# Kernel optimization log

Measured on AMD Instinct MI355X. Metric: run time of the kernel, lower is better.

## Reference

```python
import jax, jax.numpy as jnp
import numpy as np

BETA = 0.25
K = 4096
D = 256


def setup_inputs() -> dict:
    key = jax.random.key(0)
    k1, k2 = jax.random.split(key)
    z = jax.random.normal(k1, (4, D, 16, 32, 32), dtype=jnp.float32)
    # mimics nn.init.uniform_(embed.weight, -1/K, 1/K)
    embed = jax.random.uniform(k2, (K, D), minval=-1.0 / K, maxval=1.0 / K, dtype=jnp.float32)
    return {"z": z, "embed": embed}


def reference(z, embed):
    # z: [B, D, T, H, W] -> channel-last [B, T, H, W, D]
    z_perm = jnp.transpose(z, (0, 2, 3, 4, 1))
    flat = z_perm.reshape(-1, embed.shape[1])  # [N, D]
    # squared L2 distances via expansion: |z|^2 - 2 z.e + |e|^2  -> [N, K]
    dist = ((flat ** 2).sum(axis=1, keepdims=True)
            - 2.0 * flat @ embed.T
            + (embed ** 2).sum(axis=1)[None, :])
    idx = jnp.argmin(dist, axis=1)  # [N]
    z_q = embed[idx].reshape(z_perm.shape)  # [B, T, H, W, D]
    # straight-through estimator
    z_q_st = z_perm + jax.lax.stop_gradient(z_q - z_perm)
    z_q_st = jnp.transpose(z_q_st, (0, 4, 1, 2, 3))  # back to [B, D, T, H, W]
    e_q = jnp.transpose(z_q, (0, 4, 1, 2, 3))
    codebook_loss = jnp.mean((jax.lax.stop_gradient(e_q) - z) ** 2)
    commitment_loss = jnp.mean((e_q - jax.lax.stop_gradient(z)) ** 2)
    vq_loss = codebook_loss + BETA * commitment_loss
    indices = idx.reshape(z_perm.shape[:4])  # [B, T, H, W]
    return (z_q_st, vq_loss, indices)
```

## Files before the change

### kernel.cpp

```cpp
#include <hip/hip_runtime.h>
#include <float.h>

#define KC 4096
#define DIM 256
#define MB 16384
#define NTOT 65536
#define ZELEMS 16777216
#define LOSS_OFF 16777216
#define IDX_OFF  16777217
#define TAU 1.5e-4f

#define BT_OFF   524288
#define CNT_OFF  528400
#define CAND_OFF 532480
#define FULL_OFF 800000

typedef _Float16 h8 __attribute__((ext_vector_type(8)));
typedef float f4v __attribute__((ext_vector_type(4)));

__device__ __forceinline__ bool lexlt(float av, int ai, float bv, int bi) {
    return (av < bv) || (av == bv && ai < bi);
}

__global__ __launch_bounds__(256) void vq_prep(const float* __restrict__ e,
                                               float* __restrict__ out) {
    if (blockIdx.x < 512) {
        int t = blockIdx.x * 256 + threadIdx.x;
        int code = t >> 5, s8 = t & 31;
        const float4* src = reinterpret_cast<const float4*>(e + (size_t)code * DIM + s8 * 8);
        float4 v0 = src[0], v1 = src[1];
        float f[8] = {v0.x, v0.y, v0.z, v0.w, v1.x, v1.y, v1.z, v1.w};
        union { uint4 q; _Float16 h[8]; } P;
        #pragma unroll
        for (int p = 0; p < 8; ++p) P.h[p] = (_Float16)(f[p] * 4096.0f);
        int kc = s8 >> 2, khi = s8 & 3;
        int lane = khi * 16 + (code & 15);
        int slot = ((code >> 4) * 8 + kc) * 64 + lane;
        reinterpret_cast<uint4*>(out)[slot] = P.q;
    } else {
        int k = (blockIdx.x - 512) * 4 + (threadIdx.x >> 6);
        int lane = threadIdx.x & 63;
        float4 v = reinterpret_cast<const float4*>(e + (size_t)k * DIM)[lane];
        double s = (double)v.x * v.x + (double)v.y * v.y + (double)v.z * v.z + (double)v.w * v.w;
        #pragma unroll
        for (int off = 32; off > 0; off >>= 1) s += __shfl_down(s, off);
        if (lane == 0) out[BT_OFF + k] = (float)s;
    }
}

#define INS4(V0, V1, V2, V3, L0, L1, L2, L3, v, k)                              \
    if (v < V3) {                                                               \
        if (v < V2) {                                                           \
            V3 = V2; L3 = L2;                                                   \
            if (v < V1) {                                                       \
                V2 = V1; L2 = L1;                                               \
                if (v < V0) { V1 = V0; L1 = L0; V0 = v; L0 = k; }               \
                else        { V1 = v; L1 = k; }                                 \
            } else { V2 = v; L2 = k; }                                          \
        } else { V3 = v; L3 = k; }                                              \
    }

__global__ __launch_bounds__(256) void vq_fast(const float* __restrict__ z,
                                               float* __restrict__ out) {
    __shared__ uint4 etile[2][512];
    __shared__ unsigned long long lists[4][16][4];
    const int tid = threadIdx.x;
    const int wave = tid >> 6, lane = tid & 63;
    const int khi = lane >> 4, l16 = lane & 15;
    const int nbase = blockIdx.x * 64;
    const int b = nbase / MB;
    const int mbase = nbase % MB;
    const float* zb = z + (size_t)b * DIM * MB + mbase + wave * 16 + l16;

    h8 zf[8];
    #pragma unroll
    for (int kc = 0; kc < 8; ++kc) {
        h8 va;
        #pragma unroll
        for (int j = 0; j < 8; ++j)
            va[j] = (_Float16)zb[(size_t)(kc * 32 + khi * 8 + j) * MB];
        zf[kc] = va;
    }

    const uint4* ET = reinterpret_cast<const uint4*>(out);
    const float* Btab = out + BT_OFF;

    float b1 = FLT_MAX;
    int bk = 0;
    float v0 = FLT_MAX, v1 = FLT_MAX, v2 = FLT_MAX, v3 = FLT_MAX;
    int l0 = 0, l1 = 0, l2 = 0, l3 = 0;

    uint4 r0 = ET[tid], r1 = ET[tid + 256];
    for (int tile = 0; tile < KC / 16; ++tile) {
        const int cur = tile & 1;
        etile[cur][tid] = r0; etile[cur][tid + 256] = r1;
        __syncthreads();
        if (tile < KC / 16 - 1) {
            r0 = ET[(size_t)(tile + 1) * 512 + tid];
            r1 = ET[(size_t)(tile + 1) * 512 + tid + 256];
        }

        f4v ae = {0.f, 0.f, 0.f, 0.f}, ao = ae;
        #pragma unroll
        for (int kc = 0; kc < 8; kc += 2) {
            union { uint4 q; h8 v; } afe, afo;
            afe.q = etile[cur][kc * 64 + lane];
            afo.q = etile[cur][(kc + 1) * 64 + lane];
            ae = __builtin_amdgcn_mfma_f32_16x16x32_f16(afe.v, zf[kc], ae, 0, 0, 0);
            ao = __builtin_amdgcn_mfma_f32_16x16x32_f16(afo.v, zf[kc + 1], ao, 0, 0, 0);
        }

        const f4v Bv = *reinterpret_cast<const f4v*>(Btab + tile * 16 + khi * 4);
        const int kb = tile * 16 + khi * 4;
        float sc[4];
        #pragma unroll
        for (int i = 0; i < 4; ++i)
            sc[i] = fmaf(-4.8828125e-4f, ae[i] + ao[i], Bv[i]);
        float m = fminf(fminf(sc[0], sc[1]), fminf(sc[2], sc[3]));
        if (m <= b1 + TAU) {
            #pragma unroll
            for (int i = 0; i < 4; ++i) {
                float s = sc[i]; int k = kb + i;
                if (s < b1) {
                    if (b1 <= s + TAU) INS4(v0, v1, v2, v3, l0, l1, l2, l3, b1, bk)
                    b1 = s; bk = k;
                } else if (s <= b1 + TAU) {
                    INS4(v0, v1, v2, v3, l0, l1, l2, l3, s, k)
                }
            }
        }
    }

    float gb = b1;
    int gk = bk;
    #pragma unroll
    for (int off = 16; off < 64; off <<= 1) {
        float ov = __shfl_xor(gb, off); int ok = __shfl_xor(gk, off);
        if (lexlt(ov, ok, gb, gk)) { gb = ov; gk = ok; }
    }
    const float thr = gb + TAU;

    int n = 0, pa = 0, pb = 0, pc = 0, pd = 0;
    #define ADDW(kk) { if (n == 0) pa = kk; else if (n == 1) pb = kk; \
                       else if (n == 2) pc = kk; else if (n == 3) pd = kk; n++; }
    if (b1 <= thr) ADDW(bk)
    if (v0 <= thr) ADDW(l0)
    if (v1 <= thr) ADDW(l1)
    if (v2 <= thr) ADDW(l2)
    if (v3 <= thr) ADDW(l3)
    lists[wave][l16][khi] = ((unsigned long long)n << 48) |
        (unsigned long long)pa | ((unsigned long long)pb << 12) |
        ((unsigned long long)pc << 24) | ((unsigned long long)pd << 36);
    __syncthreads();

    unsigned* cntg = (unsigned*)(out + CNT_OFF);
    {
        bool act = (lane < 16);
        int gidx = nbase + wave * 16 + l16;
        int I1 = gk;
        int tot = 0, c[4];
        c[0] = c[1] = c[2] = c[3] = I1;
        if (act) {
            #pragma unroll
            for (int q = 0; q < 4; ++q) {
                unsigned long long pl = lists[wave][l16][q];
                int pcnt = (int)(pl >> 48);
                #pragma unroll
                for (int j = 0; j < 4; ++j) {
                    int kv = (int)((pl >> (12 * j)) & 4095ull);
                    if (j < pcnt && tot + j < 4) c[tot + j] = kv;
                }
                tot += pcnt;
            }
            out[IDX_OFF + gidx] = (float)I1;
        }
        bool cand = act && (tot >= 2) && (tot <= 4);
        bool full = act && (tot > 4);
        unsigned long long mc = __ballot(cand);
        if (mc) {
            int leader = __ffsll((long long)mc) - 1;
            unsigned base = 0;
            if (lane == leader) base = atomicAdd(cntg, (unsigned)__popcll(mc));
            base = __shfl(base, leader);
            if (cand) {
                unsigned pos = base + (unsigned)__popcll(mc & ((1ull << lane) - 1ull));
                reinterpret_cast<uint4*>(out + CAND_OFF)[pos] =
                    make_uint4((unsigned)gidx,
                               (unsigned)c[0] | ((unsigned)c[1] << 16),
                               (unsigned)c[2] | ((unsigned)c[3] << 16), 0u);
            }
        }
        unsigned long long mf = __ballot(full);
        if (mf) {
            int leader = __ffsll((long long)mf) - 1;
            unsigned base = 0;
            if (lane == leader) base = atomicAdd(cntg + 1, (unsigned)__popcll(mf));
            base = __shfl(base, leader);
            if (full) {
                unsigned pos = base + (unsigned)__popcll(mf & ((1ull << lane) - 1ull));
                reinterpret_cast<unsigned*>(out + FULL_OFF)[pos] = (unsigned)gidx;
            }
        }
    }
}

__global__ __launch_bounds__(256) void vq_resolve_cand(const float* __restrict__ z,
                                                       const float* __restrict__ e,
                                                       float* __restrict__ out) {
    const int wave = threadIdx.x >> 6, lane = threadIdx.x & 63;
    const unsigned n = *reinterpret_cast<const unsigned*>(out + CNT_OFF);
    const uint4* list = reinterpret_cast<const uint4*>(out + CAND_OFF);
    const float* Btab = out + BT_OFF;
    for (unsigned ei = blockIdx.x * 4 + wave; ei < n; ei += gridDim.x * 4) {
        uint4 ent = list[ei];
        const int gidx = (int)ent.x;
        const int c1 = (int)(ent.y & 0xFFFFu), c2 = (int)(ent.y >> 16);
        const int c3 = (int)(ent.z & 0xFFFFu), c4 = (int)(ent.z >> 16);
        const int b = gidx >> 14, m = gidx & (MB - 1);
        const float* zr = z + (size_t)b * DIM * MB + m;
        const float* e1 = e + (size_t)c1 * DIM;
        const float* e2 = e + (size_t)c2 * DIM;
        const float* e3 = e + (size_t)c3 * DIM;
        const float* e4 = e + (size_t)c4 * DIM;
        double A = 0.0;
        double d1 = 0.0, d2 = 0.0, d3 = 0.0, d4 = 0.0;
        #pragma unroll
        for (int jj = 0; jj < 4; ++jj) {
            int d = lane * 4 + jj;
            double zv = (double)zr[(size_t)d * MB];
            A = fma(zv, zv, A);
            d1 = fma(zv, (double)e1[d], d1);
            d2 = fma(zv, (double)e2[d], d2);
            d3 = fma(zv, (double)e3[d], d3);
            d4 = fma(zv, (double)e4[d], d4);
        }
        #pragma unroll
        for (int mm = 1; mm < 64; mm <<= 1) {
            A += __shfl_xor(A, mm);
            d1 += __shfl_xor(d1, mm); d2 += __shfl_xor(d2, mm);
            d3 += __shfl_xor(d3, mm); d4 += __shfl_xor(d4, mm);
        }
        if (lane == 0) {
            float Af = (float)A;
            float s1 = (Af - (float)(2.0 * d1)) + Btab[c1];
            float s2 = (Af - (float)(2.0 * d2)) + Btab[c2];
            float s3 = (Af - (float)(2.0 * d3)) + Btab[c3];
            float s4 = (Af - (float)(2.0 * d4)) + Btab[c4];
            float bv = s1; int bk = c1;
            if (lexlt(s2, c2, bv, bk)) { bv = s2; bk = c2; }
            if (lexlt(s3, c3, bv, bk)) { bv = s3; bk = c3; }
            if (lexlt(s4, c4, bv, bk)) { bv = s4; bk = c4; }
            out[IDX_OFF + gidx] = (float)bk;
        }
    }
}

__global__ __launch_bounds__(256) void vq_resolve_full(const float* __restrict__ z,
                                                       const float* __restrict__ e,
                                                       float* __restrict__ out) {
    __shared__ float zs[DIM];
    __shared__ float rv[4];
    __shared__ int ri[4];
    const int tid = threadIdx.x;
    const int wave = tid >> 6, lane = tid & 63;
    const unsigned n = reinterpret_cast<const unsigned*>(out + CNT_OFF)[1];
    const unsigned* list = reinterpret_cast<const unsigned*>(out + FULL_OFF);
    const float* Btab = out + BT_OFF;
    for (unsigned ei = blockIdx.x; ei < n; ei += gridDim.x) {
        const int gidx = (int)list[ei];
        const int b = gidx >> 14, m = gidx & (MB - 1);
        const float* zr = z + (size_t)b * DIM * MB + m;
        if (tid < DIM) zs[tid] = zr[(size_t)tid * MB];
        __syncthreads();
        double av = 0.0;
        #pragma unroll
        for (int t2 = 0; t2 < 4; ++t2) {
            double zv = (double)zs[lane * 4 + t2];
            av = fma(zv, zv, av);
        }
        #pragma unroll
        for (int mm = 1; mm < 64; mm <<= 1) av += __shfl_xor(av, mm);
        const float Af = (float)av;

        float bsv = FLT_MAX; int bsk = 0;
        for (int kk = 0; kk < 16; ++kk) {
            const int k = kk * 256 + tid;
            const float4* er4 = reinterpret_cast<const float4*>(e + (size_t)k * DIM);
            const float4* zs4 = reinterpret_cast<const float4*>(zs);
            double dot0 = 0.0, dot1 = 0.0;
            #pragma unroll 8
            for (int d4 = 0; d4 < 64; ++d4) {
                float4 ev = er4[d4];
                float4 zv = zs4[d4];
                dot0 = fma((double)zv.x, (double)ev.x, dot0);
                dot1 = fma((double)zv.y, (double)ev.y, dot1);
                dot0 = fma((double)zv.z, (double)ev.z, dot0);
                dot1 = fma((double)zv.w, (double)ev.w, dot1);
            }
            float s = (Af - (float)(2.0 * (dot0 + dot1))) + Btab[k];
            if (s < bsv) { bsv = s; bsk = k; }
        }
        #pragma unroll
        for (int mm = 1; mm < 64; mm <<= 1) {
            float ov = __shfl_xor(bsv, mm);
            int oi = __shfl_xor(bsk, mm);
            if (ov < bsv || (ov == bsv && oi < bsk)) { bsv = ov; bsk = oi; }
        }
        if (lane == 0) { rv[wave] = bsv; ri[wave] = bsk; }
        __syncthreads();
        if (tid == 0) {
            float bv = rv[0]; int bk = ri[0];
            #pragma unroll
            for (int wv = 1; wv < 4; ++wv) {
                if (rv[wv] < bv || (rv[wv] == bv && ri[wv] < bk)) { bv = rv[wv]; bk = ri[wv]; }
            }
            out[IDX_OFF + gidx] = (float)bk;
        }
        __syncthreads();
    }
}

__global__ __launch_bounds__(256) void vq_apply(const float* __restrict__ z,
                                                const float* __restrict__ e,
                                                float* __restrict__ out) {
    __shared__ int lds_fi[64];
    __shared__ float lds_e[64][260];
    __shared__ double lds_ls[4];
    const int tid = threadIdx.x;
    const int wave = tid >> 6, lane = tid & 63;
    const int nbase = blockIdx.x * 64;
    const int b = nbase / MB;
    const int mbase = nbase % MB;
    if (tid < 64) lds_fi[tid] = (int)out[IDX_OFF + nbase + tid];
    __syncthreads();
    for (int r = wave; r < 64; r += 4) {
        int code = lds_fi[r];
        float4 v = reinterpret_cast<const float4*>(e + (size_t)code * DIM)[lane];
        *reinterpret_cast<float4*>(&lds_e[r][lane * 4]) = v;
    }
    __syncthreads();

    double lsum = 0.0;
    const int mloc = tid & 63;
    const int d0 = tid >> 6;
    #pragma unroll 4
    for (int d = d0; d < DIM; d += 4) {
        float ev = lds_e[mloc][d];
        size_t off = (size_t)b * (DIM * MB) + (size_t)d * MB + mbase + mloc;
        float zv = z[off];
        out[off] = ev;
        float diff = ev - zv;
        lsum += (double)diff * diff;
    }
    #pragma unroll
    for (int off = 32; off > 0; off >>= 1) lsum += __shfl_down(lsum, off);
    if (lane == 0) lds_ls[wave] = lsum;
    __syncthreads();
    if (tid == 0) {
        double t = lds_ls[0] + lds_ls[1] + lds_ls[2] + lds_ls[3];
        atomicAdd(out + LOSS_OFF, (float)(t * (1.25 / (double)ZELEMS)));
    }
}

extern "C" void kernel_launch(void* const* d_in, const int* in_sizes, int n_in,
                              void* d_out, int out_size, void* d_ws, size_t ws_size,
                              hipStream_t stream) {
    const float* z = (const float*)d_in[0];
    const float* e = (const float*)d_in[1];
    float* out = (float*)d_out;

    hipMemsetAsync(out + LOSS_OFF, 0, sizeof(float), stream);
    hipMemsetAsync(out + CNT_OFF, 0, 2 * sizeof(unsigned), stream);
    vq_prep<<<1536, 256, 0, stream>>>(e, out);
    vq_fast<<<NTOT / 64, 256, 0, stream>>>(z, out);
    vq_resolve_cand<<<1024, 256, 0, stream>>>(z, e, out);
    vq_resolve_full<<<512, 256, 0, stream>>>(z, e, out);
    vq_apply<<<NTOT / 64, 256, 0, stream>>>(z, e, out);
}
```

Baseline: 427.7 us.

## Double codebook tile per sync in vq_fast and halve vq_apply block size

```diff
diff --git a/kernel.cpp b/kernel.cpp
--- a/kernel.cpp
+++ b/kernel.cpp
@@ -62,7 +62,7 @@
 
 __global__ __launch_bounds__(256) void vq_fast(const float* __restrict__ z,
                                                float* __restrict__ out) {
-    __shared__ uint4 etile[2][512];
+    __shared__ uint4 etile[2][1024];
     __shared__ unsigned long long lists[4][16][4];
     const int tid = threadIdx.x;
     const int wave = tid >> 6, lane = tid & 63;
@@ -90,37 +90,59 @@
     float v0 = FLT_MAX, v1 = FLT_MAX, v2 = FLT_MAX, v3 = FLT_MAX;
     int l0 = 0, l1 = 0, l2 = 0, l3 = 0;
 
-    uint4 r0 = ET[tid], r1 = ET[tid + 256];
-    for (int tile = 0; tile < KC / 16; ++tile) {
+    uint4 r0 = ET[tid], r1 = ET[tid + 256], r2 = ET[tid + 512], r3 = ET[tid + 768];
+    for (int tile = 0; tile < KC / 32; ++tile) {
         const int cur = tile & 1;
         etile[cur][tid] = r0; etile[cur][tid + 256] = r1;
+        etile[cur][tid + 512] = r2; etile[cur][tid + 768] = r3;
         __syncthreads();
-        if (tile < KC / 16 - 1) {
-            r0 = ET[(size_t)(tile + 1) * 512 + tid];
-            r1 = ET[(size_t)(tile + 1) * 512 + tid + 256];
-        }
-
-        f4v ae = {0.f, 0.f, 0.f, 0.f}, ao = ae;
+        if (tile < KC / 32 - 1) {
+            size_t base = (size_t)(tile + 1) * 1024;
+            r0 = ET[base + tid];       r1 = ET[base + tid + 256];
+            r2 = ET[base + tid + 512]; r3 = ET[base + tid + 768];
+        }
+
+        f4v a0e = {0.f, 0.f, 0.f, 0.f}, a0o = a0e, a1e = a0e, a1o = a0e;
         #pragma unroll
         for (int kc = 0; kc < 8; kc += 2) {
-            union { uint4 q; h8 v; } afe, afo;
-            afe.q = etile[cur][kc * 64 + lane];
-            afo.q = etile[cur][(kc + 1) * 64 + lane];
-            ae = __builtin_amdgcn_mfma_f32_16x16x32_f16(afe.v, zf[kc], ae, 0, 0, 0);
-            ao = __builtin_amdgcn_mfma_f32_16x16x32_f16(afo.v, zf[kc + 1], ao, 0, 0, 0);
-        }
-
-        const f4v Bv = *reinterpret_cast<const f4v*>(Btab + tile * 16 + khi * 4);
-        const int kb = tile * 16 + khi * 4;
-        float sc[4];
-        #pragma unroll
-        for (int i = 0; i < 4; ++i)
-            sc[i] = fmaf(-4.8828125e-4f, ae[i] + ao[i], Bv[i]);
-        float m = fminf(fminf(sc[0], sc[1]), fminf(sc[2], sc[3]));
-        if (m <= b1 + TAU) {
+            union { uint4 q; h8 v; } f0e, f0o, f1e, f1o;
+            f0e.q = etile[cur][kc * 64 + lane];
+            f0o.q = etile[cur][(kc + 1) * 64 + lane];
+            f1e.q = etile[cur][512 + kc * 64 + lane];
+            f1o.q = etile[cur][512 + (kc + 1) * 64 + lane];
+            a0e = __builtin_amdgcn_mfma_f32_16x16x32_f16(f0e.v, zf[kc], a0e, 0, 0, 0);
+            a0o = __builtin_amdgcn_mfma_f32_16x16x32_f16(f0o.v, zf[kc + 1], a0o, 0, 0, 0);
+            a1e = __builtin_amdgcn_mfma_f32_16x16x32_f16(f1e.v, zf[kc], a1e, 0, 0, 0);
+            a1o = __builtin_amdgcn_mfma_f32_16x16x32_f16(f1o.v, zf[kc + 1], a1o, 0, 0, 0);
+        }
+
+        const f4v Bv0 = *reinterpret_cast<const f4v*>(Btab + tile * 32 + khi * 4);
+        const f4v Bv1 = *reinterpret_cast<const f4v*>(Btab + tile * 32 + 16 + khi * 4);
+        const int kb0 = tile * 32 + khi * 4;
+        float sc0[4], sc1[4];
+        #pragma unroll
+        for (int i = 0; i < 4; ++i) {
+            sc0[i] = fmaf(-4.8828125e-4f, a0e[i] + a0o[i], Bv0[i]);
+            sc1[i] = fmaf(-4.8828125e-4f, a1e[i] + a1o[i], Bv1[i]);
+        }
+        float m0 = fminf(fminf(sc0[0], sc0[1]), fminf(sc0[2], sc0[3]));
+        if (m0 <= b1 + TAU) {
             #pragma unroll
             for (int i = 0; i < 4; ++i) {
-                float s = sc[i]; int k = kb + i;
+                float s = sc0[i]; int k = kb0 + i;
+                if (s < b1) {
+                    if (b1 <= s + TAU) INS4(v0, v1, v2, v3, l0, l1, l2, l3, b1, bk)
+                    b1 = s; bk = k;
+                } else if (s <= b1 + TAU) {
+                    INS4(v0, v1, v2, v3, l0, l1, l2, l3, s, k)
+                }
+            }
+        }
+        float m1 = fminf(fminf(sc1[0], sc1[1]), fminf(sc1[2], sc1[3]));
+        if (m1 <= b1 + TAU) {
+            #pragma unroll
+            for (int i = 0; i < 4; ++i) {
+                float s = sc1[i]; int k = kb0 + 16 + i;
                 if (s < b1) {
                     if (b1 <= s + TAU) INS4(v0, v1, v2, v3, l0, l1, l2, l3, b1, bk)
                     b1 = s; bk = k;
@@ -323,17 +345,17 @@
 __global__ __launch_bounds__(256) void vq_apply(const float* __restrict__ z,
                                                 const float* __restrict__ e,
                                                 float* __restrict__ out) {
-    __shared__ int lds_fi[64];
-    __shared__ float lds_e[64][260];
+    __shared__ int lds_fi[32];
+    __shared__ float lds_e[32][260];
     __shared__ double lds_ls[4];
     const int tid = threadIdx.x;
     const int wave = tid >> 6, lane = tid & 63;
-    const int nbase = blockIdx.x * 64;
+    const int nbase = blockIdx.x * 32;
     const int b = nbase / MB;
     const int mbase = nbase % MB;
-    if (tid < 64) lds_fi[tid] = (int)out[IDX_OFF + nbase + tid];
+    if (tid < 32) lds_fi[tid] = (int)out[IDX_OFF + nbase + tid];
     __syncthreads();
-    for (int r = wave; r < 64; r += 4) {
+    for (int r = wave; r < 32; r += 4) {
         int code = lds_fi[r];
         float4 v = reinterpret_cast<const float4*>(e + (size_t)code * DIM)[lane];
         *reinterpret_cast<float4*>(&lds_e[r][lane * 4]) = v;
@@ -341,10 +363,10 @@
     __syncthreads();
 
     double lsum = 0.0;
-    const int mloc = tid & 63;
-    const int d0 = tid >> 6;
+    const int mloc = tid & 31;
+    const int d0 = tid >> 5;
     #pragma unroll 4
-    for (int d = d0; d < DIM; d += 4) {
+    for (int d = d0; d < DIM; d += 8) {
         float ev = lds_e[mloc][d];
         size_t off = (size_t)b * (DIM * MB) + (size_t)d * MB + mbase + mloc;
         float zv = z[off];
@@ -375,5 +397,5 @@
     vq_fast<<<NTOT / 64, 256, 0, stream>>>(z, out);
     vq_resolve_cand<<<1024, 256, 0, stream>>>(z, e, out);
     vq_resolve_full<<<512, 256, 0, stream>>>(z, e, out);
-    vq_apply<<<NTOT / 64, 256, 0, stream>>>(z, e, out);
-}
+    vq_apply<<<NTOT / 32, 256, 0, stream>>>(z, e, out);
+}
```

New measurement: 518.3 us. +21.2%, slower.
